# Kernel optimization log

Hardware: AMD Instinct MI355X
Metric: run time of the kernel (lower is better)

The kernel has to match this reference:

```python
import jax, jax.numpy as jnp
import numpy as np

N_SRC0, N_DST0, N_E0 = 286000, 11000, 275000
N_DST1, N_E1 = 1000, 10000
IN_FEATS, N_HIDDEN, N_CLASSES = 602, 256, 41


def setup_inputs() -> dict:
    key = jax.random.key(0)
    ks = jax.random.split(key, 12)
    inp = {
        "x": jax.random.normal(ks[0], (N_SRC0, IN_FEATS), dtype=jnp.float32),
        "Wself0": jax.random.normal(ks[1], (IN_FEATS, N_HIDDEN), dtype=jnp.float32) * 0.05,
        "Wneigh0": jax.random.normal(ks[2], (IN_FEATS, N_HIDDEN), dtype=jnp.float32) * 0.05,
        "b0": jnp.zeros((N_HIDDEN,), dtype=jnp.float32),
        "Wself1": jax.random.normal(ks[3], (N_HIDDEN, N_CLASSES), dtype=jnp.float32) * 0.05,
        "Wneigh1": jax.random.normal(ks[4], (N_HIDDEN, N_CLASSES), dtype=jnp.float32) * 0.05,
        "b1": jnp.zeros((N_CLASSES,), dtype=jnp.float32),
        "e0_src": jax.random.randint(ks[5], (N_E0,), 0, N_SRC0, dtype=jnp.int64 if jax.config.jax_enable_x64 else jnp.int32),
        "e0_dst": jax.random.randint(ks[6], (N_E0,), 0, N_DST0, dtype=jnp.int64 if jax.config.jax_enable_x64 else jnp.int32),
        "e1_src": jax.random.randint(ks[7], (N_E1,), 0, N_DST0, dtype=jnp.int64 if jax.config.jax_enable_x64 else jnp.int32),
        "e1_dst": jax.random.randint(ks[8], (N_E1,), 0, N_DST1, dtype=jnp.int64 if jax.config.jax_enable_x64 else jnp.int32),
    }
    return inp


def _mean_agg(h, src, dst, n_dst):
    # gather neighbor feats along edges, segment-mean into dst nodes
    s = jax.ops.segment_sum(h[src], dst, num_segments=n_dst)  # [n_dst, d]
    cnt = jax.ops.segment_sum(jnp.ones_like(dst, dtype=h.dtype), dst, num_segments=n_dst)
    return s / jnp.maximum(cnt, 1.0)[:, None]


def reference(x, Wself0, Wneigh0, b0, Wself1, Wneigh1, b1, e0_src, e0_dst, e1_src, e1_dst):
    # Layer 0: SAGEConv mean over block0 (src=286000, dst=11000) + relu
    # (dropout is identity in eval mode)
    h_dst = x[:N_DST0]
    h_agg = _mean_agg(x, e0_src, e0_dst, N_DST0)
    h = h_dst @ Wself0 + h_agg @ Wneigh0 + b0
    h = jax.nn.relu(h)
    # Layer 1: SAGEConv mean over block1 (src=11000, dst=1000)
    h_dst1 = h[:N_DST1]
    h_agg1 = _mean_agg(h, e1_src, e1_dst, N_DST1)
    out = h_dst1 @ Wself1 + h_agg1 @ Wneigh1 + b1
    return out
```

## Files before the change

kernel.cpp:

```cpp
#include <hip/hip_runtime.h>

#define N_SRC0   286000
#define N_DST0   11000
#define N_E0     275000
#define N_DST1   1000
#define N_E1     10000
#define IN_FEATS 602
#define N_HIDDEN 256
#define N_CLASSES 41


__global__ void count_kernel(const int* __restrict__ d0, int n0, int* __restrict__ c0,
                             const int* __restrict__ d1, int n1, int* __restrict__ c1) {
    int i = blockIdx.x * blockDim.x + threadIdx.x;
    if (i < n0) {
        atomicAdd(&c0[d0[i]], 1);
    } else {
        int j = i - n0;
        if (j < n1) atomicAdd(&c1[d1[j]], 1);
    }
}

__global__ void scan_kernel(const int* __restrict__ cnt0, int* __restrict__ off0, int n0_,
                            const int* __restrict__ cnt1, int* __restrict__ off1, int n1_) {
    const int* cnt; int* off; int n;
    if (blockIdx.x == 0) { cnt = cnt0; off = off0; n = n0_; }
    else                 { cnt = cnt1; off = off1; n = n1_; }
    __shared__ int sums[1024];
    int tid = threadIdx.x;
    int chunk = (n + 1023) >> 10;
    int start = tid * chunk;
    int end = min(start + chunk, n);
    int s = 0;
    for (int i = start; i < end; i++) s += cnt[i];
    sums[tid] = s;
    __syncthreads();
    for (int d = 1; d < 1024; d <<= 1) {
        int v = (tid >= d) ? sums[tid - d] : 0;
        __syncthreads();
        sums[tid] += v;
        __syncthreads();
    }
    int run = (tid > 0) ? sums[tid - 1] : 0;
    for (int i = start; i < end; i++) { off[i] = run; run += cnt[i]; }
    if (tid == 1023) off[n] = run;
}

__global__ void fill_kernel(const int* __restrict__ s0, const int* __restrict__ d0, int n0,
                            const int* __restrict__ off0, int* __restrict__ cur0, int* __restrict__ csr0,
                            const int* __restrict__ s1, const int* __restrict__ d1, int n1,
                            const int* __restrict__ off1, int* __restrict__ cur1, int* __restrict__ csr1) {
    int i = blockIdx.x * blockDim.x + threadIdx.x;
    if (i < n0) {
        int d = d0[i];
        int p = atomicAdd(&cur0[d], 1);
        csr0[off0[d] + p] = s0[i];
    } else {
        int j = i - n0;
        if (j < n1) {
            int d = d1[j];
            int p = atomicAdd(&cur1[d], 1);
            csr1[off1[d] + p] = s1[j];
        }
    }
}

__global__ void agg0_kernel(const float* __restrict__ x, const int* __restrict__ off,
                            const int* __restrict__ csr, float* __restrict__ agg) {
    int d = blockIdx.x;
    int tid = threadIdx.x;
    int c0 = tid, c1 = tid + 256, c2 = tid + 512;
    bool has2 = (c2 < IN_FEATS);
    float a0 = 0.f, a1 = 0.f, a2 = 0.f;
    int beg = off[d], end = off[d + 1];
    int e = beg;
    for (; e + 1 < end; e += 2) {
        const float* r0 = x + (size_t)csr[e] * IN_FEATS;
        const float* r1 = x + (size_t)csr[e + 1] * IN_FEATS;
        float t00 = r0[c0], t01 = r0[c1];
        float t10 = r1[c0], t11 = r1[c1];
        float t02 = has2 ? r0[c2] : 0.f;
        float t12 = has2 ? r1[c2] : 0.f;
        a0 += t00 + t10;
        a1 += t01 + t11;
        a2 += t02 + t12;
    }
    if (e < end) {
        const float* r0 = x + (size_t)csr[e] * IN_FEATS;
        a0 += r0[c0];
        a1 += r0[c1];
        if (has2) a2 += r0[c2];
    }
    float inv = 1.f / fmaxf((float)(end - beg), 1.f);
    float* o = agg + (size_t)d * IN_FEATS;
    o[c0] = a0 * inv;
    o[c1] = a1 * inv;
    if (has2) o[c2] = a2 * inv;
}

#define BM 64
#define BN 64
#define BK 16
#define TM 4
#define TN 4
#define LDA (BM + 4)

__global__ __launch_bounds__(256) void layer0_kernel(
        const float* __restrict__ x, const float* __restrict__ agg,
        const float* __restrict__ Wself, const float* __restrict__ Wneigh,
        const float* __restrict__ b, float* __restrict__ h) {
    __shared__ float As[BK][LDA];
    __shared__ float Bs[BK][BN];
    const int t  = threadIdx.x;
    const int tx = t & 15;
    const int ty = t >> 4;
    const int row0 = blockIdx.x * BM;
    const int col0 = blockIdx.y * BN;

    float acc[TM][TN];
#pragma unroll
    for (int m = 0; m < TM; m++)
#pragma unroll
        for (int n = 0; n < TN; n++) acc[m][n] = 0.f;

    for (int part = 0; part < 2; part++) {
        const float* A = part ? agg : x;
        const float* W = part ? Wneigh : Wself;
        for (int k0 = 0; k0 < IN_FEATS; k0 += BK) {
#pragma unroll
            for (int l = 0; l < (BM * BK) / 256; l++) {
                int idx = t + l * 256;
                int i = idx / BK, k = idx % BK;
                int gr = row0 + i, gk = k0 + k;
                As[k][i] = (gr < N_DST0 && gk < IN_FEATS) ? A[(size_t)gr * IN_FEATS + gk] : 0.f;
            }
#pragma unroll
            for (int l = 0; l < (BK * BN) / 256; l++) {
                int idx = t + l * 256;
                int k = idx / BN, n = idx % BN;
                int gk = k0 + k;
                Bs[k][n] = (gk < IN_FEATS) ? W[(size_t)gk * N_HIDDEN + col0 + n] : 0.f;
            }
            __syncthreads();
#pragma unroll
            for (int k = 0; k < BK; k++) {
                float4 av = *(const float4*)&As[k][ty * TM];
                float4 bv = *(const float4*)&Bs[k][tx * TN];
                float a[TM] = {av.x, av.y, av.z, av.w};
                float bb[TN] = {bv.x, bv.y, bv.z, bv.w};
#pragma unroll
                for (int m = 0; m < TM; m++)
#pragma unroll
                    for (int n = 0; n < TN; n++) acc[m][n] += a[m] * bb[n];
            }
            __syncthreads();
        }
    }
#pragma unroll
    for (int m = 0; m < TM; m++) {
        int gr = row0 + ty * TM + m;
        if (gr < N_DST0) {
#pragma unroll
            for (int n = 0; n < TN; n++) {
                int gc = col0 + tx * TN + n;
                h[(size_t)gr * N_HIDDEN + gc] = fmaxf(acc[m][n] + b[gc], 0.f);
            }
        }
    }
}

__global__ void agg1_kernel(const float* __restrict__ h, const int* __restrict__ off,
                            const int* __restrict__ csr, float* __restrict__ agg) {
    int d = blockIdx.x;
    int tid = threadIdx.x;
    float a = 0.f;
    int beg = off[d], end = off[d + 1];
    for (int e = beg; e < end; e++)
        a += h[(size_t)csr[e] * N_HIDDEN + tid];
    agg[(size_t)d * N_HIDDEN + tid] = a / fmaxf((float)(end - beg), 1.f);
}

__global__ void layer1_kernel(const float* __restrict__ h, const float* __restrict__ agg1,
                              const float* __restrict__ Wself, const float* __restrict__ Wneigh,
                              const float* __restrict__ b, float* __restrict__ out) {
    int idx = blockIdx.x * blockDim.x + threadIdx.x;
    if (idx >= N_DST1 * N_CLASSES) return;
    int d = idx / N_CLASSES, c = idx % N_CLASSES;
    const float* hd = h + (size_t)d * N_HIDDEN;
    const float* ha = agg1 + (size_t)d * N_HIDDEN;
    float acc = b[c];
    for (int k = 0; k < N_HIDDEN; k++)
        acc += hd[k] * Wself[k * N_CLASSES + c] + ha[k] * Wneigh[k * N_CLASSES + c];
    out[idx] = acc;
}

extern "C" void kernel_launch(void* const* d_in, const int* in_sizes, int n_in,
                              void* d_out, int out_size, void* d_ws, size_t ws_size,
                              hipStream_t stream) {
    const float* x       = (const float*)d_in[0];
    const float* Wself0  = (const float*)d_in[1];
    const float* Wneigh0 = (const float*)d_in[2];
    const float* b0      = (const float*)d_in[3];
    const float* Wself1  = (const float*)d_in[4];
    const float* Wneigh1 = (const float*)d_in[5];
    const float* b1      = (const float*)d_in[6];
    const int* e0_src = (const int*)d_in[7];
    const int* e0_dst = (const int*)d_in[8];
    const int* e1_src = (const int*)d_in[9];
    const int* e1_dst = (const int*)d_in[10];

    char* ws = (char*)d_ws;
    size_t o = 0;
    auto alloc = [&](size_t bytes) -> void* {
        void* p = ws + o;
        o = (o + bytes + 255) & ~(size_t)255;
        return p;
    };
    int* cnt_block = (int*)alloc((size_t)(N_DST0 + N_DST0 + N_DST1 + N_DST1) * sizeof(int));
    int* cnt0 = cnt_block;
    int* cur0 = cnt_block + N_DST0;
    int* cnt1 = cnt_block + 2 * N_DST0;
    int* cur1 = cnt_block + 2 * N_DST0 + N_DST1;
    int* off0 = (int*)alloc((size_t)(N_DST0 + 1) * sizeof(int));
    int* off1 = (int*)alloc((size_t)(N_DST1 + 1) * sizeof(int));
    int* csr0 = (int*)alloc((size_t)N_E0 * sizeof(int));
    int* csr1 = (int*)alloc((size_t)N_E1 * sizeof(int));
    float* agg0 = (float*)alloc((size_t)N_DST0 * IN_FEATS * sizeof(float));
    float* h    = (float*)alloc((size_t)N_DST0 * N_HIDDEN * sizeof(float));
    float* agg1 = (float*)alloc((size_t)N_DST1 * N_HIDDEN * sizeof(float));

    hipMemsetAsync(cnt_block, 0, (size_t)(2 * N_DST0 + 2 * N_DST1) * sizeof(int), stream);

    int total_e = N_E0 + N_E1;
    count_kernel<<<(total_e + 255) / 256, 256, 0, stream>>>(e0_dst, N_E0, cnt0, e1_dst, N_E1, cnt1);
    scan_kernel<<<2, 1024, 0, stream>>>(cnt0, off0, N_DST0, cnt1, off1, N_DST1);
    fill_kernel<<<(total_e + 255) / 256, 256, 0, stream>>>(e0_src, e0_dst, N_E0, off0, cur0, csr0,
                                                           e1_src, e1_dst, N_E1, off1, cur1, csr1);
    agg0_kernel<<<N_DST0, 256, 0, stream>>>(x, off0, csr0, agg0);
    dim3 g0((N_DST0 + BM - 1) / BM, N_HIDDEN / BN);
    layer0_kernel<<<g0, 256, 0, stream>>>(x, agg0, Wself0, Wneigh0, b0, h);
    agg1_kernel<<<N_DST1, 256, 0, stream>>>(h, off1, csr1, agg1);
    layer1_kernel<<<(N_DST1 * N_CLASSES + 255) / 256, 256, 0, stream>>>(h, agg1, Wself1, Wneigh1, b1,
                                                                        (float*)d_out);
}
```

Measured before the change: 1.198 ms.

## Use split-bf16 MFMA for layer-0 GEMM with pre-converted padded operands

Replaces the scalar FP32 tiled GEMM for layer 0 with a bf16 MFMA kernel. FP32 accuracy is kept by splitting each value into hi and lo bf16 parts and issuing three MFMAs (hi*hi, hi*lo, lo*hi). New conversion kernels pad x and the weights to K=608, storing the weights transposed. The aggregation kernel now writes split bf16 output directly and unrolls its edge loop by four. This adds conversion passes and extra memory traffic, and the padded rows beyond N_DST0 in the workspace are read without being initialised.

New measurement: 1.001 ms. -16.5%, faster.

```diff
diff --git a/kernel.cpp b/kernel.cpp
--- a/kernel.cpp
+++ b/kernel.cpp
@@ -8,6 +8,25 @@
 #define IN_FEATS 602
 #define N_HIDDEN 256
 #define N_CLASSES 41
+
+#define KP 608
+#define MP 11008
+#define LDT 40
+
+typedef unsigned short u16;
+typedef __attribute__((ext_vector_type(8))) short short8;
+typedef __attribute__((ext_vector_type(4))) float f32x4;
+
+__device__ inline void split_bf16(float v, u16& hi, u16& lo) {
+    unsigned u = __float_as_uint(v);
+    unsigned r = u + 0x7FFFu + ((u >> 16) & 1u);
+    hi = (u16)(r >> 16);
+    float vhi = __uint_as_float((unsigned)hi << 16);
+    float vl = v - vhi;
+    unsigned u2 = __float_as_uint(vl);
+    unsigned r2 = u2 + 0x7FFFu + ((u2 >> 16) & 1u);
+    lo = (u16)(r2 >> 16);
+}
 
 
 __global__ void count_kernel(const int* __restrict__ d0, int n0, int* __restrict__ c0,
@@ -65,8 +84,34 @@
     }
 }
 
+__global__ void xconv_kernel(const float* __restrict__ x,
+                             u16* __restrict__ xhi, u16* __restrict__ xlo) {
+    int idx = blockIdx.x * blockDim.x + threadIdx.x;
+    if (idx >= N_DST0 * KP) return;
+    int row = idx / KP, k = idx - row * KP;
+    float v = (k < IN_FEATS) ? x[(size_t)row * IN_FEATS + k] : 0.f;
+    u16 hi, lo; split_bf16(v, hi, lo);
+    xhi[idx] = hi; xlo[idx] = lo;
+}
+
+__global__ void wconv_kernel(const float* __restrict__ Wself, const float* __restrict__ Wneigh,
+                             u16* __restrict__ wt) {
+    int idx = blockIdx.x * blockDim.x + threadIdx.x;
+    if (idx >= 2 * KP * 256) return;
+    int part = idx / (KP * 256);
+    int rem  = idx - part * (KP * 256);
+    int k = rem / 256;
+    int n = rem - k * 256;
+    float v = (k < IN_FEATS) ? (part ? Wneigh[(size_t)k * 256 + n] : Wself[(size_t)k * 256 + n]) : 0.f;
+    u16 hi, lo; split_bf16(v, hi, lo);
+    u16* base = wt + (size_t)part * 2 * 256 * KP;
+    base[(size_t)n * KP + k] = hi;
+    base[(size_t)256 * KP + (size_t)n * KP + k] = lo;
+}
+
 __global__ void agg0_kernel(const float* __restrict__ x, const int* __restrict__ off,
-                            const int* __restrict__ csr, float* __restrict__ agg) {
+                            const int* __restrict__ csr,
+                            u16* __restrict__ ahi, u16* __restrict__ alo) {
     int d = blockIdx.x;
     int tid = threadIdx.x;
     int c0 = tid, c1 = tid + 256, c2 = tid + 512;
@@ -74,96 +119,102 @@
     float a0 = 0.f, a1 = 0.f, a2 = 0.f;
     int beg = off[d], end = off[d + 1];
     int e = beg;
-    for (; e + 1 < end; e += 2) {
-        const float* r0 = x + (size_t)csr[e] * IN_FEATS;
+    for (; e + 3 < end; e += 4) {
+        const float* r0 = x + (size_t)csr[e]     * IN_FEATS;
         const float* r1 = x + (size_t)csr[e + 1] * IN_FEATS;
-        float t00 = r0[c0], t01 = r0[c1];
-        float t10 = r1[c0], t11 = r1[c1];
-        float t02 = has2 ? r0[c2] : 0.f;
-        float t12 = has2 ? r1[c2] : 0.f;
-        a0 += t00 + t10;
-        a1 += t01 + t11;
-        a2 += t02 + t12;
-    }
-    if (e < end) {
+        const float* r2 = x + (size_t)csr[e + 2] * IN_FEATS;
+        const float* r3 = x + (size_t)csr[e + 3] * IN_FEATS;
+        float t00 = r0[c0], t10 = r1[c0], t20 = r2[c0], t30 = r3[c0];
+        float t01 = r0[c1], t11 = r1[c1], t21 = r2[c1], t31 = r3[c1];
+        float t02 = has2 ? r0[c2] : 0.f, t12 = has2 ? r1[c2] : 0.f;
+        float t22 = has2 ? r2[c2] : 0.f, t32 = has2 ? r3[c2] : 0.f;
+        a0 += (t00 + t10) + (t20 + t30);
+        a1 += (t01 + t11) + (t21 + t31);
+        a2 += (t02 + t12) + (t22 + t32);
+    }
+    for (; e < end; e++) {
         const float* r0 = x + (size_t)csr[e] * IN_FEATS;
         a0 += r0[c0];
         a1 += r0[c1];
         if (has2) a2 += r0[c2];
     }
     float inv = 1.f / fmaxf((float)(end - beg), 1.f);
-    float* o = agg + (size_t)d * IN_FEATS;
-    o[c0] = a0 * inv;
-    o[c1] = a1 * inv;
-    if (has2) o[c2] = a2 * inv;
-}
-
-#define BM 64
-#define BN 64
-#define BK 16
-#define TM 4
-#define TN 4
-#define LDA (BM + 4)
-
-__global__ __launch_bounds__(256) void layer0_kernel(
-        const float* __restrict__ x, const float* __restrict__ agg,
-        const float* __restrict__ Wself, const float* __restrict__ Wneigh,
-        const float* __restrict__ b, float* __restrict__ h) {
-    __shared__ float As[BK][LDA];
-    __shared__ float Bs[BK][BN];
-    const int t  = threadIdx.x;
-    const int tx = t & 15;
-    const int ty = t >> 4;
-    const int row0 = blockIdx.x * BM;
-    const int col0 = blockIdx.y * BN;
-
-    float acc[TM][TN];
-#pragma unroll
-    for (int m = 0; m < TM; m++)
-#pragma unroll
-        for (int n = 0; n < TN; n++) acc[m][n] = 0.f;
+    size_t base = (size_t)d * KP;
+    u16 hi, lo;
+    split_bf16(a0 * inv, hi, lo); ahi[base + c0] = hi; alo[base + c0] = lo;
+    split_bf16(a1 * inv, hi, lo); ahi[base + c1] = hi; alo[base + c1] = lo;
+    if (c2 < KP) {
+        float v = has2 ? a2 * inv : 0.f;
+        split_bf16(v, hi, lo); ahi[base + c2] = hi; alo[base + c2] = lo;
+    }
+}
+
+__global__ __launch_bounds__(256) void layer0_mfma(
+        const u16* __restrict__ xhi, const u16* __restrict__ xlo,
+        const u16* __restrict__ ghi, const u16* __restrict__ glo,
+        const u16* __restrict__ wt, const float* __restrict__ b,
+        float* __restrict__ h) {
+    __shared__ u16 Ahi[64][LDT], Alo[64][LDT], Bhi[64][LDT], Blo[64][LDT];
+    const int t    = threadIdx.x;
+    const int lane = t & 63;
+    const int w    = t >> 6;
+    const int wm   = w >> 1, wn = w & 1;
+    const int row0 = blockIdx.x * 64;
+    const int col0 = blockIdx.y * 64;
+    const int sr   = t >> 2;
+    const int sc   = (t & 3) * 8;
+    const int fr   = lane & 15;
+    const int ko   = (lane >> 4) * 8;
+
+    f32x4 acc[2][2] = {};
 
     for (int part = 0; part < 2; part++) {
-        const float* A = part ? agg : x;
-        const float* W = part ? Wneigh : Wself;
-        for (int k0 = 0; k0 < IN_FEATS; k0 += BK) {
-#pragma unroll
-            for (int l = 0; l < (BM * BK) / 256; l++) {
-                int idx = t + l * 256;
-                int i = idx / BK, k = idx % BK;
-                int gr = row0 + i, gk = k0 + k;
-                As[k][i] = (gr < N_DST0 && gk < IN_FEATS) ? A[(size_t)gr * IN_FEATS + gk] : 0.f;
+        const u16* Aphi = part ? ghi : xhi;
+        const u16* Aplo = part ? glo : xlo;
+        const u16* Bphi = wt + (size_t)part * 2 * 256 * KP;
+        const u16* Bplo = Bphi + (size_t)256 * KP;
+        for (int k0 = 0; k0 < KP; k0 += 32) {
+            short8 va = *reinterpret_cast<const short8*>(&Aphi[(size_t)(row0 + sr) * KP + k0 + sc]);
+            short8 vb = *reinterpret_cast<const short8*>(&Aplo[(size_t)(row0 + sr) * KP + k0 + sc]);
+            short8 vc = *reinterpret_cast<const short8*>(&Bphi[(size_t)(col0 + sr) * KP + k0 + sc]);
+            short8 vd = *reinterpret_cast<const short8*>(&Bplo[(size_t)(col0 + sr) * KP + k0 + sc]);
+            __syncthreads();
+            *reinterpret_cast<short8*>(&Ahi[sr][sc]) = va;
+            *reinterpret_cast<short8*>(&Alo[sr][sc]) = vb;
+            *reinterpret_cast<short8*>(&Bhi[sr][sc]) = vc;
+            *reinterpret_cast<short8*>(&Blo[sr][sc]) = vd;
+            __syncthreads();
+            short8 bh[2], bl[2];
+#pragma unroll
+            for (int n = 0; n < 2; n++) {
+                bh[n] = *reinterpret_cast<const short8*>(&Bhi[wn * 32 + n * 16 + fr][ko]);
+                bl[n] = *reinterpret_cast<const short8*>(&Blo[wn * 32 + n * 16 + fr][ko]);
             }
 #pragma unroll
-            for (int l = 0; l < (BK * BN) / 256; l++) {
-                int idx = t + l * 256;
-                int k = idx / BN, n = idx % BN;
-                int gk = k0 + k;
-                Bs[k][n] = (gk < IN_FEATS) ? W[(size_t)gk * N_HIDDEN + col0 + n] : 0.f;
+            for (int m = 0; m < 2; m++) {
+                short8 ah = *reinterpret_cast<const short8*>(&Ahi[wm * 32 + m * 16 + fr][ko]);
+                short8 al = *reinterpret_cast<const short8*>(&Alo[wm * 32 + m * 16 + fr][ko]);
+#pragma unroll
+                for (int n = 0; n < 2; n++) {
+                    acc[m][n] = __builtin_amdgcn_mfma_f32_16x16x32_bf16(ah, bh[n], acc[m][n], 0, 0, 0);
+                    acc[m][n] = __builtin_amdgcn_mfma_f32_16x16x32_bf16(ah, bl[n], acc[m][n], 0, 0, 0);
+                    acc[m][n] = __builtin_amdgcn_mfma_f32_16x16x32_bf16(al, bh[n], acc[m][n], 0, 0, 0);
+                }
             }
-            __syncthreads();
-#pragma unroll
-            for (int k = 0; k < BK; k++) {
-                float4 av = *(const float4*)&As[k][ty * TM];
-                float4 bv = *(const float4*)&Bs[k][tx * TN];
-                float a[TM] = {av.x, av.y, av.z, av.w};
-                float bb[TN] = {bv.x, bv.y, bv.z, bv.w};
-#pragma unroll
-                for (int m = 0; m < TM; m++)
-#pragma unroll
-                    for (int n = 0; n < TN; n++) acc[m][n] += a[m] * bb[n];
-            }
-            __syncthreads();
         }
     }
-#pragma unroll
-    for (int m = 0; m < TM; m++) {
-        int gr = row0 + ty * TM + m;
-        if (gr < N_DST0) {
-#pragma unroll
-            for (int n = 0; n < TN; n++) {
-                int gc = col0 + tx * TN + n;
-                h[(size_t)gr * N_HIDDEN + gc] = fmaxf(acc[m][n] + b[gc], 0.f);
+    const int fq = lane >> 4;
+#pragma unroll
+    for (int m = 0; m < 2; m++) {
+#pragma unroll
+        for (int n = 0; n < 2; n++) {
+            int gcol = col0 + wn * 32 + n * 16 + fr;
+            float bc = b[gcol];
+#pragma unroll
+            for (int r = 0; r < 4; r++) {
+                int grow = row0 + wm * 32 + m * 16 + fq * 4 + r;
+                if (grow < N_DST0)
+                    h[(size_t)grow * N_HIDDEN + gcol] = fmaxf(acc[m][n][r] + bc, 0.f);
             }
         }
     }
@@ -225,7 +276,11 @@
     int* off1 = (int*)alloc((size_t)(N_DST1 + 1) * sizeof(int));
     int* csr0 = (int*)alloc((size_t)N_E0 * sizeof(int));
     int* csr1 = (int*)alloc((size_t)N_E1 * sizeof(int));
-    float* agg0 = (float*)alloc((size_t)N_DST0 * IN_FEATS * sizeof(float));
+    u16* xhi = (u16*)alloc((size_t)MP * KP * sizeof(u16));
+    u16* xlo = (u16*)alloc((size_t)MP * KP * sizeof(u16));
+    u16* ahi = (u16*)alloc((size_t)MP * KP * sizeof(u16));
+    u16* alo = (u16*)alloc((size_t)MP * KP * sizeof(u16));
+    u16* wt  = (u16*)alloc((size_t)2 * 2 * 256 * KP * sizeof(u16));
     float* h    = (float*)alloc((size_t)N_DST0 * N_HIDDEN * sizeof(float));
     float* agg1 = (float*)alloc((size_t)N_DST1 * N_HIDDEN * sizeof(float));
 
@@ -236,9 +291,11 @@
     scan_kernel<<<2, 1024, 0, stream>>>(cnt0, off0, N_DST0, cnt1, off1, N_DST1);
     fill_kernel<<<(total_e + 255) / 256, 256, 0, stream>>>(e0_src, e0_dst, N_E0, off0, cur0, csr0,
                                                            e1_src, e1_dst, N_E1, off1, cur1, csr1);
-    agg0_kernel<<<N_DST0, 256, 0, stream>>>(x, off0, csr0, agg0);
-    dim3 g0((N_DST0 + BM - 1) / BM, N_HIDDEN / BN);
-    layer0_kernel<<<g0, 256, 0, stream>>>(x, agg0, Wself0, Wneigh0, b0, h);
+    xconv_kernel<<<(N_DST0 * KP + 255) / 256, 256, 0, stream>>>(x, xhi, xlo);
+    wconv_kernel<<<(2 * KP * 256 + 255) / 256, 256, 0, stream>>>(Wself0, Wneigh0, wt);
+    agg0_kernel<<<N_DST0, 256, 0, stream>>>(x, off0, csr0, ahi, alo);
+    dim3 g0(MP / 64, N_HIDDEN / 64);
+    layer0_mfma<<<g0, 256, 0, stream>>>(xhi, xlo, ahi, alo, wt, b0, h);
     agg1_kernel<<<N_DST1, 256, 0, stream>>>(h, off1, csr1, agg1);
     layer1_kernel<<<(N_DST1 * N_CLASSES + 255) / 256, 256, 0, stream>>>(h, agg1, Wself1, Wneigh1, b1,
                                                                         (float*)d_out);
```
